# Kernel tuning notes

Hardware: AMD Instinct MI355X
Metric: run time of the kernel (lower is better)

The kernel has to match this reference:

```python
import jax, jax.numpy as jnp
from jax import lax
import numpy as np

B, H, W = 16, 512, 512
NBINS = 256
MARGIN_EYE = 12
BLUR_SIZE = 5
ALPHA_SKIN, ALPHA_EYE, ALPHA_LIP = 0.3, 0.8, 0.1


def de_norm(x):
    return jnp.clip((x + 1.0) * 0.5, 0.0, 1.0)


def renorm(x):
    return x * 2.0 - 1.0


def _match_channel(src, ref, w_s, w_r):
    # src/ref: (P,) pixel values in [0,255]; w_s/w_r: (P,) mask weights
    b_s = jnp.clip(src.astype(jnp.int32), 0, NBINS - 1)
    b_r = jnp.clip(ref.astype(jnp.int32), 0, NBINS - 1)
    h_s = jnp.zeros((NBINS,), src.dtype).at[b_s].add(w_s)   # masked histogram
    h_r = jnp.zeros((NBINS,), ref.dtype).at[b_r].add(w_r)
    cdf_s = jnp.cumsum(h_s) / jnp.maximum(jnp.sum(h_s), 1e-6)
    cdf_r = jnp.cumsum(h_r) / jnp.maximum(jnp.sum(h_r), 1e-6)
    # CDF-matching transfer table (equiv. of cal_trans in PSGAN/EleGANt)
    table = jnp.clip(jnp.searchsorted(cdf_r, cdf_s), 0, NBINS - 1).astype(src.dtype)
    return table[b_s]


def masked_his_match(image_s, image_r, mask_s, mask_r):
    # image: (3,H,W), mask: (1,H,W)
    s = de_norm(image_s) * 255.0 * mask_s
    r = de_norm(image_r) * 255.0 * mask_r
    w_s = mask_s.reshape(-1)
    w_r = mask_r.reshape(-1)
    matched = jax.vmap(_match_channel, in_axes=(0, 0, None, None))(
        s.reshape(3, -1), r.reshape(3, -1), w_s, w_r).reshape(s.shape)
    matched = jnp.where(mask_s > 0, matched, s)  # only masked pixels replaced
    return renorm(matched / 255.0)


def expand_area(mask, margin):
    # morphological dilation (max pool) of (1,H,W) mask
    k = 2 * margin + 1
    return lax.reduce_window(mask, 0.0, lax.max, (1, k, k), (1, 1, 1), 'SAME')


def mask_blur(mask, blur_size):
    # box blur; 'valid' mode: blurred support kept inside original mask
    k = blur_size
    s = lax.reduce_window(mask, 0.0, lax.add, (1, k, k), (1, 1, 1), 'SAME') / float(k * k)
    return s * mask


def generate_pgt(image_s, image_r, mask_s, mask_r, lms_s, lms_r):
    pgt = image_s
    # skin (channel 1)
    m = mask_s[1:2]
    pgt = (1.0 - m) * pgt + m * masked_his_match(image_s, image_r, m, mask_r[1:2])
    # neck (channel 4)
    m = mask_s[4:5]
    pgt = (1.0 - m) * pgt + m * masked_his_match(image_s, image_r, m, mask_r[4:5])
    # lip (channel 0)
    m = mask_s[0:1]
    pgt = (1.0 - m) * pgt + m * masked_his_match(image_s, image_r, m, mask_r[0:1])
    # eyes (channels 2,3), dilated and intersected with skin
    m_se = expand_area(jnp.sum(mask_s[2:4], axis=0, keepdims=True), MARGIN_EYE) * mask_s[1:2]
    m_re = expand_area(jnp.sum(mask_r[2:4], axis=0, keepdims=True), MARGIN_EYE) * mask_r[1:2]
    eye_match = masked_his_match(image_s, image_r, m_se, m_re)
    mb = mask_blur(m_se, BLUR_SIZE)
    pgt = (1.0 - mb) * pgt + mb * eye_match
    # fine_align (reconstructed, simplified: per-region alpha blend of reference,
    # landmark warp omitted -- helper source not provided)
    for m, a in ((mask_s[1:2], ALPHA_SKIN), (m_se, ALPHA_EYE), (mask_s[0:1], ALPHA_LIP)):
        pgt = (1.0 - a * m) * pgt + (a * m) * image_r
    return pgt


def setup_inputs() -> dict:
    key = jax.random.key(0)
    ks = jax.random.split(key, 6)
    sources = jax.random.uniform(ks[0], (B, 3, H, W), jnp.float32, -1.0, 1.0)
    targets = jax.random.uniform(ks[1], (B, 3, H, W), jnp.float32, -1.0, 1.0)
    mask_srcs = (jax.random.uniform(ks[2], (B, 5, H, W)) < 0.3).astype(jnp.float32)
    mask_tars = (jax.random.uniform(ks[3], (B, 5, H, W)) < 0.3).astype(jnp.float32)
    lms_srcs = jax.random.uniform(ks[4], (B, 68, 2), jnp.float32, 0.0, float(H))
    lms_tars = jax.random.uniform(ks[5], (B, 68, 2), jnp.float32, 0.0, float(H))
    return {"sources": sources, "targets": targets, "mask_srcs": mask_srcs,
            "mask_tars": mask_tars, "lms_srcs": lms_srcs, "lms_tars": lms_tars}


def reference(sources, targets, mask_srcs, mask_tars, lms_srcs, lms_tars):
    # vmap over batch replaces the per-sample Python loop of ComposePGT.forward
    return jax.vmap(generate_pgt)(sources, targets, mask_srcs, mask_tars, lms_srcs, lms_tars)
```

## Files before the change

### kernel.cpp

```cpp
#include <hip/hip_runtime.h>
#include <stdint.h>

#define BB 16
#define HH 512
#define WW 512
#define HW (HH*WW)
#define NB 256


__device__ __forceinline__ float denorm255(float x) {
    return fminf(fmaxf((x + 1.0f) * 0.5f, 0.0f), 1.0f) * 255.0f;
}
__device__ __forceinline__ float renorm_lut(int t) {
    return ((float)t / 255.0f) * 2.0f - 1.0f;
}
__device__ __forceinline__ uint32_t alignb(uint32_t hi, uint32_t lo, int r) {
    return (uint32_t)(((((uint64_t)hi) << 32) | lo) >> (8 * r));
}

__global__ void __launch_bounds__(256, 4) prep_hor_kernel(
    const float* __restrict__ ms, const float* __restrict__ mr,
    uint32_t* __restrict__ C, uint32_t* __restrict__ eh)
{
    int blk  = blockIdx.x;
    int side = blk >> 10;
    int rem  = blk & 1023;
    int b    = rem >> 6;
    int rg   = rem & 63;
    int r    = threadIdx.x >> 5;
    int c    = threadIdx.x & 31;
    int y    = (rg << 3) + r;

    const float* base = (side ? mr : ms) + (size_t)b * 5 * HW + (size_t)y * WW;

    float4 v[5][4];
    #pragma unroll
    for (int p = 0; p < 5; p++) {
        const float4* pp = (const float4*)(base + (size_t)p * HW);
        #pragma unroll
        for (int j = 0; j < 4; j++) v[p][j] = pp[4 * c + j];
    }

    uint32_t Wd[4], E[4];
    #pragma unroll
    for (int j = 0; j < 4; j++) {
        uint32_t wc = 0;
        #pragma unroll
        for (int k = 0; k < 4; k++) {
            float a0 = (&v[0][j].x)[k];
            float a1 = (&v[1][j].x)[k];
            float a2 = (&v[2][j].x)[k];
            float a3 = (&v[3][j].x)[k];
            float a4 = (&v[4][j].x)[k];
            uint32_t e  = (uint32_t)(a2 + a3);
            uint32_t pb = (a0 > 0.f ? 4u : 0u) | (a1 > 0.f ? 8u : 0u)
                        | (a4 > 0.f ? 16u : 0u);
            wc |= (e | pb) << (8 * k);
        }
        Wd[j] = wc;
        E[j]  = wc & 0x03030303u;
    }

    size_t plane = (size_t)(side * BB + b);
    uint32_t* Crow = C + plane * (HW / 4) + y * 128;
    *((uint4*)(Crow + 4 * c)) = make_uint4(Wd[0], Wd[1], Wd[2], Wd[3]);

    uint32_t Lw[3], Rw[3];
    #pragma unroll
    for (int i = 0; i < 3; i++) {
        uint32_t lv = __shfl_up(E[i + 1], 1, 32);
        Lw[i] = (c == 0) ? 0u : lv;
        uint32_t rv = __shfl_down(E[i], 1, 32);
        Rw[i] = (c == 31) ? 0u : rv;
    }
    uint32_t arr[10] = {Lw[0], Lw[1], Lw[2], E[0], E[1], E[2], E[3],
                        Rw[0], Rw[1], Rw[2]};

    uint32_t acc[4];
    #pragma unroll
    for (int k = 0; k < 4; k++) {
        const int b3 = 3 + k;
        uint32_t a = arr[b3];
        #pragma unroll
        for (int s = 1; s <= 12; s++) {
            int ai = s >> 2, rr = s & 3;
            uint32_t vp, vm;
            if (rr == 0) {
                vp = arr[b3 + ai];
                vm = arr[b3 - ai];
            } else {
                vp = alignb(arr[b3 + ai + 1], arr[b3 + ai], rr);
                int am = (s + 3) >> 2;
                vm = alignb(arr[b3 - am + 1], arr[b3 - am], 4 - rr);
            }
            a |= vp | vm;
        }
        acc[k] = a;
    }
    uint32_t* Erow = eh + plane * (HW / 4) + y * 128;
    *((uint4*)(Erow + 4 * c)) = make_uint4(acc[0], acc[1], acc[2], acc[3]);
}

__global__ void __launch_bounds__(256) ver_kernel(
    const uint32_t* __restrict__ eh, uint32_t* __restrict__ C)
{
    int t   = blockIdx.x * 256 + threadIdx.x;
    int sb  = t >> 12;
    int rem = t & 4095;
    int yg  = rem >> 5;
    int ck  = rem & 31;
    int y0  = yg << 2;
    const uint4* P = (const uint4*)(eh + (size_t)sb * (HW / 4));
    auto R = [&](int y) -> uint4 {
        uint4 z = {0, 0, 0, 0};
        if (y < 0 || y >= HH) return z;
        return P[y * 32 + ck];
    };
    uint4 core = {0, 0, 0, 0};
    #pragma unroll
    for (int yy = -9; yy <= 12; yy++) {
        uint4 r = R(y0 + yy);
        core.x |= r.x; core.y |= r.y; core.z |= r.z; core.w |= r.w;
    }
    uint4 b0 = R(y0 - 12), b1 = R(y0 - 11), b2 = R(y0 - 10);
    uint4 a0 = R(y0 + 13), a1 = R(y0 + 14), a2 = R(y0 + 15);

    uint4* C4 = (uint4*)(C + (size_t)sb * (HW / 4));
    #pragma unroll
    for (int i = 0; i < 4; i++) {
        uint4 v = core;
        if (i == 0) { v.x|=b0.x|b1.x|b2.x; v.y|=b0.y|b1.y|b2.y; v.z|=b0.z|b1.z|b2.z; v.w|=b0.w|b1.w|b2.w; }
        if (i == 1) { v.x|=b1.x|b2.x|a0.x; v.y|=b1.y|b2.y|a0.y; v.z|=b1.z|b2.z|a0.z; v.w|=b1.w|b2.w|a0.w; }
        if (i == 2) { v.x|=b2.x|a0.x|a1.x; v.y|=b2.y|a0.y|a1.y; v.z|=b2.z|a0.z|a1.z; v.w|=b2.w|a0.w|a1.w; }
        if (i == 3) { v.x|=a0.x|a1.x|a2.x; v.y|=a0.y|a1.y|a2.y; v.z|=a0.z|a1.z|a2.z; v.w|=a0.w|a1.w|a2.w; }
        int idx = (y0 + i) * 32 + ck;
        uint4 cw = C4[idx];
        #pragma unroll
        for (int q = 0; q < 4; q++) {
            uint32_t vv = (&v.x)[q];
            uint32_t cc = (&cw.x)[q];
            uint32_t t3 = vv & (vv >> 1) & 0x01010101u;
            vv -= t3;
            uint32_t m1b = (cc >> 3) & 0x01010101u;
            vv &= m1b * 255u;
            (&cw.x)[q] = cc | (vv << 5);
        }
        C4[idx] = cw;
    }
}

__global__ void __launch_bounds__(256) blur_kernel(
    const uint32_t* __restrict__ C, uint4* __restrict__ mbs)
{
    int t = blockIdx.x * 256 + threadIdx.x;
    int b = t >> 14;
    int rem = t & 16383;
    int y = rem >> 5;
    int c = rem & 31;
    const uint32_t* P = C + (size_t)b * (HW / 4);
    int c4 = c << 2;
    uint32_t s[6] = {0u, 0u, 0u, 0u, 0u, 0u};
    #pragma unroll
    for (int dy = -2; dy <= 2; dy++) {
        int yy = y + dy;
        if (yy < 0 || yy >= HH) continue;
        const uint32_t* rp = P + yy * 128;
        uint32_t l = (c > 0)  ? rp[c4 - 1] : 0u;
        uint4 m = *((const uint4*)(rp + c4));
        uint32_t rr = (c < 31) ? rp[c4 + 4] : 0u;
        s[0] += (l   >> 5) & 0x03030303u;
        s[1] += (m.x >> 5) & 0x03030303u;
        s[2] += (m.y >> 5) & 0x03030303u;
        s[3] += (m.z >> 5) & 0x03030303u;
        s[4] += (m.w >> 5) & 0x03030303u;
        s[5] += (rr  >> 5) & 0x03030303u;
    }
    uint4 o;
    #pragma unroll
    for (int k = 0; k < 4; k++) {
        uint32_t v = s[k + 1];
        v += alignb(s[k + 1], s[k],     2);
        v += alignb(s[k + 1], s[k],     3);
        v += alignb(s[k + 2], s[k + 1], 1);
        v += alignb(s[k + 2], s[k + 1], 2);
        (&o.x)[k] = v;
    }
    mbs[t] = o;
}

#define HB 32
__device__ __forceinline__ void hist4(int* h, uint32_t cw,
                                      float4 v0, float4 v1, float4 v2)
{
    float d0[4] = {denorm255(v0.x), denorm255(v0.y), denorm255(v0.z), denorm255(v0.w)};
    float d1[4] = {denorm255(v1.x), denorm255(v1.y), denorm255(v1.z), denorm255(v1.w)};
    float d2[4] = {denorm255(v2.x), denorm255(v2.y), denorm255(v2.z), denorm255(v2.w)};
    #pragma unroll
    for (int j = 0; j < 4; j++) {
        uint32_t pb = (cw >> (8 * j)) & 0xFFu;
        if (pb & 8u) {
            atomicAdd(&h[0 * NB + min((int)d0[j], 255)], 1);
            atomicAdd(&h[1 * NB + min((int)d1[j], 255)], 1);
            atomicAdd(&h[2 * NB + min((int)d2[j], 255)], 1);
        }
        if (pb & 16u) {
            atomicAdd(&h[3 * NB + min((int)d0[j], 255)], 1);
            atomicAdd(&h[4 * NB + min((int)d1[j], 255)], 1);
            atomicAdd(&h[5 * NB + min((int)d2[j], 255)], 1);
        }
        if (pb & 4u) {
            atomicAdd(&h[6 * NB + min((int)d0[j], 255)], 1);
            atomicAdd(&h[7 * NB + min((int)d1[j], 255)], 1);
            atomicAdd(&h[8 * NB + min((int)d2[j], 255)], 1);
        }
        int mei = (int)((pb >> 5) & 3u);
        if (mei) {
            float fm = (float)mei;
            atomicAdd(&h[ 9 * NB + min((int)(d0[j] * fm), 255)], mei);
            atomicAdd(&h[10 * NB + min((int)(d1[j] * fm), 255)], mei);
            atomicAdd(&h[11 * NB + min((int)(d2[j] * fm), 255)], mei);
        }
    }
}

__global__ void __launch_bounds__(256) hist_kernel(
    const float* __restrict__ src, const float* __restrict__ tgt,
    const uint32_t* __restrict__ C, int* __restrict__ hist)
{
    int bs  = blockIdx.x / HB;
    int blk = blockIdx.x % HB;
    int b = bs >> 1, side = bs & 1;
    const float* img = (side ? tgt : src) + (size_t)b * 3 * HW;
    const float4* i0 = (const float4*)(img);
    const float4* i1 = (const float4*)(img + HW);
    const float4* i2 = (const float4*)(img + 2 * (size_t)HW);
    const uint2* pc = (const uint2*)(C + (size_t)(side * BB + b) * (HW / 4));

    __shared__ int h[2][12 * NB];
    int* hw = h[threadIdx.x >> 7];
    for (int i = threadIdx.x; i < 2 * 12 * NB; i += 256) ((int*)h)[i] = 0;
    __syncthreads();

    for (int c = blk * 256 + threadIdx.x; c < HW / 8; c += HB * 256) {
        uint2 cw = pc[c];
        float4 a0 = i0[2 * c], b0 = i0[2 * c + 1];
        float4 a1 = i1[2 * c], b1 = i1[2 * c + 1];
        float4 a2 = i2[2 * c], b2 = i2[2 * c + 1];
        hist4(hw, cw.x, a0, a1, a2);
        hist4(hw, cw.y, b0, b1, b2);
    }
    __syncthreads();
    int* gh = hist + (size_t)bs * 12 * NB;
    for (int i = threadIdx.x; i < 12 * NB; i += 256) {
        int s = h[0][i] + h[1][i];
        if (s) atomicAdd(&gh[i], s);
    }
}

__global__ void __launch_bounds__(NB) table_kernel(
    const int* __restrict__ hist, uint8_t* __restrict__ table)
{
    int idx = blockIdx.x;
    int c = idx % 3; int rest = idx / 3; int rg = rest & 3; int b = rest >> 2;
    const int* hs = hist + ((size_t)((b * 2 + 0) * 4 + rg) * 3 + c) * NB;
    const int* hr = hist + ((size_t)((b * 2 + 1) * 4 + rg) * 3 + c) * NB;
    __shared__ int a[NB];
    __shared__ float cr[NB];
    int t = threadIdx.x;

    a[t] = hs[t];
    __syncthreads();
    for (int off = 1; off < NB; off <<= 1) {
        int v = (t >= off) ? a[t - off] : 0;
        __syncthreads();
        a[t] += v;
        __syncthreads();
    }
    int totS = a[NB - 1];
    int cumS = a[t];
    __syncthreads();

    a[t] = hr[t];
    __syncthreads();
    for (int off = 1; off < NB; off <<= 1) {
        int v = (t >= off) ? a[t - off] : 0;
        __syncthreads();
        a[t] += v;
        __syncthreads();
    }
    int totR = a[NB - 1];
    cr[t] = (float)a[t] / fmaxf((float)totR, 1e-6f);
    float v = (float)cumS / fmaxf((float)totS, 1e-6f);
    __syncthreads();

    int cnt = 0;
    for (int j = 0; j < NB; j++) cnt += (cr[j] < v) ? 1 : 0;
    table[(size_t)idx * NB + t] = (uint8_t)min(cnt, 255);
}

__device__ __forceinline__ void proc4(uint32_t cw, uint32_t qw,
    float4 x0, float4 x1, float4 x2, float4 r0, float4 r1, float4 r2,
    const uint8_t* tb, float4& o0, float4& o1, float4& o2)
{
    float X0[4] = {x0.x, x0.y, x0.z, x0.w};
    float X1[4] = {x1.x, x1.y, x1.z, x1.w};
    float X2[4] = {x2.x, x2.y, x2.z, x2.w};
    float R0[4] = {r0.x, r0.y, r0.z, r0.w};
    float R1[4] = {r1.x, r1.y, r1.z, r1.w};
    float R2[4] = {r2.x, r2.y, r2.z, r2.w};
    #pragma unroll
    for (int j = 0; j < 4; j++) {
        uint32_t pb = (cw >> (8 * j)) & 0xFFu;
        float q = (float)((qw >> (8 * j)) & 0xFFu);
        float m0f = (float)((pb >> 2) & 1u);
        float m1f = (float)((pb >> 3) & 1u);
        float m4f = (float)((pb >> 4) & 1u);
        float fm  = (float)((pb >> 5) & 3u);
        float d0 = denorm255(X0[j]), d1 = denorm255(X1[j]), d2 = denorm255(X2[j]);
        float p0 = X0[j], p1 = X1[j], p2 = X2[j];
        {
            float e0 = renorm_lut(tb[0 * NB + min((int)(d0 * m1f), 255)]);
            float e1 = renorm_lut(tb[1 * NB + min((int)(d1 * m1f), 255)]);
            float e2 = renorm_lut(tb[2 * NB + min((int)(d2 * m1f), 255)]);
            p0 = (1.0f - m1f) * p0 + m1f * e0;
            p1 = (1.0f - m1f) * p1 + m1f * e1;
            p2 = (1.0f - m1f) * p2 + m1f * e2;
        }
        {
            float e0 = renorm_lut(tb[3 * NB + min((int)(d0 * m4f), 255)]);
            float e1 = renorm_lut(tb[4 * NB + min((int)(d1 * m4f), 255)]);
            float e2 = renorm_lut(tb[5 * NB + min((int)(d2 * m4f), 255)]);
            p0 = (1.0f - m4f) * p0 + m4f * e0;
            p1 = (1.0f - m4f) * p1 + m4f * e1;
            p2 = (1.0f - m4f) * p2 + m4f * e2;
        }
        {
            float e0 = renorm_lut(tb[6 * NB + min((int)(d0 * m0f), 255)]);
            float e1 = renorm_lut(tb[7 * NB + min((int)(d1 * m0f), 255)]);
            float e2 = renorm_lut(tb[8 * NB + min((int)(d2 * m0f), 255)]);
            p0 = (1.0f - m0f) * p0 + m0f * e0;
            p1 = (1.0f - m0f) * p1 + m0f * e1;
            p2 = (1.0f - m0f) * p2 + m0f * e2;
        }
        {
            float mb = (q * (1.0f / 25.0f)) * fm;
            float e0 = renorm_lut(tb[ 9 * NB + min((int)(d0 * fm), 255)]);
            float e1 = renorm_lut(tb[10 * NB + min((int)(d1 * fm), 255)]);
            float e2 = renorm_lut(tb[11 * NB + min((int)(d2 * fm), 255)]);
            p0 = (1.0f - mb) * p0 + mb * e0;
            p1 = (1.0f - mb) * p1 + mb * e1;
            p2 = (1.0f - mb) * p2 + mb * e2;
        }
        float a = 0.3f * m1f;
        p0 = (1.0f - a) * p0 + a * R0[j];
        p1 = (1.0f - a) * p1 + a * R1[j];
        p2 = (1.0f - a) * p2 + a * R2[j];
        a = 0.8f * fm;
        p0 = (1.0f - a) * p0 + a * R0[j];
        p1 = (1.0f - a) * p1 + a * R1[j];
        p2 = (1.0f - a) * p2 + a * R2[j];
        a = 0.1f * m0f;
        p0 = (1.0f - a) * p0 + a * R0[j];
        p1 = (1.0f - a) * p1 + a * R1[j];
        p2 = (1.0f - a) * p2 + a * R2[j];
        (&o0.x)[j] = p0; (&o1.x)[j] = p1; (&o2.x)[j] = p2;
    }
}

__global__ void __launch_bounds__(256) compose_kernel(
    const float* __restrict__ src, const float* __restrict__ tgt,
    const uint32_t* __restrict__ C, const uint32_t* __restrict__ mbs,
    const uint8_t* __restrict__ table, float* __restrict__ out)
{
    int t = blockIdx.x * 256 + threadIdx.x;
    int b = t >> 15;
    int c = t & 32767;

    __shared__ uint8_t tb[12 * NB];
    {
        const uint32_t* gt = (const uint32_t*)(table + (size_t)b * 12 * NB);
        uint32_t* tw = (uint32_t*)tb;
        for (int i = threadIdx.x; i < 12 * NB / 4; i += 256) tw[i] = gt[i];
    }
    __syncthreads();

    const float4* s0 = (const float4*)(src + (size_t)b * 3 * HW);
    const float4* s1 = s0 + HW / 4;
    const float4* s2 = s1 + HW / 4;
    const float4* t0 = (const float4*)(tgt + (size_t)b * 3 * HW);
    const float4* t1 = t0 + HW / 4;
    const float4* t2 = t1 + HW / 4;
    const uint2* pc = (const uint2*)(C + (size_t)b * (HW / 4));
    const uint2* qc = (const uint2*)(mbs + (size_t)b * (HW / 4));
    float4* o0 = (float4*)(out + (size_t)b * 3 * HW);
    float4* o1 = o0 + HW / 4;
    float4* o2 = o1 + HW / 4;

    uint2 cw = pc[c];
    uint2 qw = qc[c];
    float4 xa0 = s0[2 * c], xb0 = s0[2 * c + 1];
    float4 xa1 = s1[2 * c], xb1 = s1[2 * c + 1];
    float4 xa2 = s2[2 * c], xb2 = s2[2 * c + 1];
    float4 ra0 = t0[2 * c], rb0 = t0[2 * c + 1];
    float4 ra1 = t1[2 * c], rb1 = t1[2 * c + 1];
    float4 ra2 = t2[2 * c], rb2 = t2[2 * c + 1];

    float4 oa0, oa1, oa2, ob0, ob1, ob2;
    proc4(cw.x, qw.x, xa0, xa1, xa2, ra0, ra1, ra2, tb, oa0, oa1, oa2);
    proc4(cw.y, qw.y, xb0, xb1, xb2, rb0, rb1, rb2, tb, ob0, ob1, ob2);

    o0[2 * c] = oa0; o0[2 * c + 1] = ob0;
    o1[2 * c] = oa1; o1[2 * c + 1] = ob1;
    o2[2 * c] = oa2; o2[2 * c + 1] = ob2;
}

extern "C" void kernel_launch(void* const* d_in, const int* in_sizes, int n_in,
                              void* d_out, int out_size, void* d_ws, size_t ws_size,
                              hipStream_t stream) {
    const float* src = (const float*)d_in[0];
    const float* tgt = (const float*)d_in[1];
    const float* ms  = (const float*)d_in[2];
    const float* mr  = (const float*)d_in[3];
    float* out = (float*)d_out;

    uint8_t* ws = (uint8_t*)d_ws;
    uint32_t* C   = (uint32_t*)(ws);
    uint32_t* eh  = (uint32_t*)(ws + (size_t)2 * BB * HW);
    uint32_t* mbs = (uint32_t*)(ws + (size_t)4 * BB * HW);
    int* hist     = (int*)(ws + (size_t)5 * BB * HW);
    uint8_t* table = ws + (size_t)5 * BB * HW + (size_t)2 * BB * 12 * NB * 4;

    hipMemsetAsync(hist, 0, (size_t)2 * BB * 12 * NB * sizeof(int), stream);

    prep_hor_kernel<<<2 * BB * 64, 256, 0, stream>>>(ms, mr, C, eh);
    ver_kernel<<<2 * BB * (HH / 4) * (WW / 16) / 256, 256, 0, stream>>>(eh, C);
    blur_kernel<<<BB * (HW / 16) / 256, 256, 0, stream>>>(C, (uint4*)mbs);
    hist_kernel<<<2 * BB * HB, 256, 0, stream>>>(src, tgt, C, hist);
    table_kernel<<<BB * 4 * 3, NB, 0, stream>>>(hist, table);
    compose_kernel<<<BB * (HW / 8) / 256, 256, 0, stream>>>(src, tgt, C, mbs, table, out);
}
```

Before: 330.7 us.

## Fuse mask prep, vertical dilation and blur into one LDS-tiled kernel

Replaces the three mask kernels (horizontal prep and dilation, vertical dilation, box blur) with one kernel. Each block handles a 36-row strip plus halo in shared memory, so the intermediate eh buffer and the re-read of C are no longer written to and read from global memory. It also skips loading mask planes that the halo rows do not need. The price is redundant halo loads and computation, only 480 blocks with large LDS use, and a blockIdx swizzle.

```diff
diff --git a/kernel.cpp b/kernel.cpp
--- a/kernel.cpp
+++ b/kernel.cpp
@@ -7,6 +7,11 @@
 #define HW (HH*WW)
 #define NB 256
 
+#define YC 36
+#define SROWS 64
+#define MROWS 40
+#define NYCH 15
+
 
 __device__ __forceinline__ float denorm255(float x) {
     return fminf(fmaxf((x + 1.0f) * 0.5f, 0.0f), 1.0f) * 255.0f;
@@ -18,174 +23,171 @@
     return (uint32_t)(((((uint64_t)hi) << 32) | lo) >> (8 * r));
 }
 
-__global__ void __launch_bounds__(256, 4) prep_hor_kernel(
+__global__ void __launch_bounds__(256) fused_mask_kernel(
     const float* __restrict__ ms, const float* __restrict__ mr,
-    uint32_t* __restrict__ C, uint32_t* __restrict__ eh)
-{
-    int blk  = blockIdx.x;
-    int side = blk >> 10;
-    int rem  = blk & 1023;
-    int b    = rem >> 6;
-    int rg   = rem & 63;
-    int r    = threadIdx.x >> 5;
-    int c    = threadIdx.x & 31;
-    int y    = (rg << 3) + r;
-
-    const float* base = (side ? mr : ms) + (size_t)b * 5 * HW + (size_t)y * WW;
-
-    float4 v[5][4];
-    #pragma unroll
-    for (int p = 0; p < 5; p++) {
-        const float4* pp = (const float4*)(base + (size_t)p * HW);
+    uint32_t* __restrict__ C, uint32_t* __restrict__ mbs)
+{
+    __shared__ uint32_t sHor[SROWS][128];
+    __shared__ uint32_t sMse[MROWS][129];
+
+    int blk  = (blockIdx.x & 7) * 60 + (blockIdx.x >> 3);
+    int ych  = blk % NYCH;
+    int sb   = blk / NYCH;
+    int side = sb >> 4;
+    int b    = sb & 15;
+    int y0   = ych * YC;
+
+    const float* base = (side ? mr : ms) + (size_t)b * 5 * HW;
+    int r0 = threadIdx.x >> 5;
+    int c  = threadIdx.x & 31;
+
+    for (int it = 0; it < 8; ++it) {
+        int L  = r0 + 8 * it;
+        int gy = y0 - 14 + L;
+        bool inimg = (gy >= 0 && gy < HH);
+        bool m1row = inimg && (L >= 12 && L < 52);
+        bool owned = inimg && (L >= 14 && L < 50);
+
+        float4 v[5][4];
         #pragma unroll
-        for (int j = 0; j < 4; j++) v[p][j] = pp[4 * c + j];
-    }
-
-    uint32_t Wd[4], E[4];
-    #pragma unroll
-    for (int j = 0; j < 4; j++) {
-        uint32_t wc = 0;
+        for (int p = 0; p < 5; p++)
+            #pragma unroll
+            for (int j = 0; j < 4; j++) v[p][j] = make_float4(0.f, 0.f, 0.f, 0.f);
+
+        const float* rowp = base + (size_t)gy * WW + 16 * c;
+        if (inimg) {
+            const float4* p2 = (const float4*)(rowp + 2 * (size_t)HW);
+            const float4* p3 = (const float4*)(rowp + 3 * (size_t)HW);
+            #pragma unroll
+            for (int j = 0; j < 4; j++) { v[2][j] = p2[j]; v[3][j] = p3[j]; }
+            if (m1row) {
+                const float4* p1 = (const float4*)(rowp + (size_t)HW);
+                #pragma unroll
+                for (int j = 0; j < 4; j++) v[1][j] = p1[j];
+            }
+            if (owned) {
+                const float4* p0 = (const float4*)(rowp);
+                const float4* p4 = (const float4*)(rowp + 4 * (size_t)HW);
+                #pragma unroll
+                for (int j = 0; j < 4; j++) { v[0][j] = p0[j]; v[4][j] = p4[j]; }
+            }
+        }
+
+        uint32_t Wd[4], E[4];
+        #pragma unroll
+        for (int j = 0; j < 4; j++) {
+            uint32_t wc = 0;
+            #pragma unroll
+            for (int k = 0; k < 4; k++) {
+                float a0 = (&v[0][j].x)[k];
+                float a1 = (&v[1][j].x)[k];
+                float a2 = (&v[2][j].x)[k];
+                float a3 = (&v[3][j].x)[k];
+                float a4 = (&v[4][j].x)[k];
+                uint32_t e  = (uint32_t)(a2 + a3);
+                uint32_t pb = (a0 > 0.f ? 4u : 0u) | (a1 > 0.f ? 8u : 0u)
+                            | (a4 > 0.f ? 16u : 0u);
+                wc |= (e | pb) << (8 * k);
+            }
+            Wd[j] = wc;
+            E[j]  = wc & 0x03030303u;
+        }
+
+        uint32_t Lw[3], Rw[3];
+        #pragma unroll
+        for (int i = 0; i < 3; i++) {
+            uint32_t lv = __shfl_up(E[i + 1], 1, 32);
+            Lw[i] = (c == 0) ? 0u : lv;
+            uint32_t rv = __shfl_down(E[i], 1, 32);
+            Rw[i] = (c == 31) ? 0u : rv;
+        }
+        uint32_t arr[10] = {Lw[0], Lw[1], Lw[2], E[0], E[1], E[2], E[3],
+                            Rw[0], Rw[1], Rw[2]};
         #pragma unroll
         for (int k = 0; k < 4; k++) {
-            float a0 = (&v[0][j].x)[k];
-            float a1 = (&v[1][j].x)[k];
-            float a2 = (&v[2][j].x)[k];
-            float a3 = (&v[3][j].x)[k];
-            float a4 = (&v[4][j].x)[k];
-            uint32_t e  = (uint32_t)(a2 + a3);
-            uint32_t pb = (a0 > 0.f ? 4u : 0u) | (a1 > 0.f ? 8u : 0u)
-                        | (a4 > 0.f ? 16u : 0u);
-            wc |= (e | pb) << (8 * k);
-        }
-        Wd[j] = wc;
-        E[j]  = wc & 0x03030303u;
-    }
-
-    size_t plane = (size_t)(side * BB + b);
-    uint32_t* Crow = C + plane * (HW / 4) + y * 128;
-    *((uint4*)(Crow + 4 * c)) = make_uint4(Wd[0], Wd[1], Wd[2], Wd[3]);
-
-    uint32_t Lw[3], Rw[3];
-    #pragma unroll
-    for (int i = 0; i < 3; i++) {
-        uint32_t lv = __shfl_up(E[i + 1], 1, 32);
-        Lw[i] = (c == 0) ? 0u : lv;
-        uint32_t rv = __shfl_down(E[i], 1, 32);
-        Rw[i] = (c == 31) ? 0u : rv;
-    }
-    uint32_t arr[10] = {Lw[0], Lw[1], Lw[2], E[0], E[1], E[2], E[3],
-                        Rw[0], Rw[1], Rw[2]};
-
-    uint32_t acc[4];
-    #pragma unroll
-    for (int k = 0; k < 4; k++) {
-        const int b3 = 3 + k;
-        uint32_t a = arr[b3];
-        #pragma unroll
-        for (int s = 1; s <= 12; s++) {
-            int ai = s >> 2, rr = s & 3;
-            uint32_t vp, vm;
-            if (rr == 0) {
-                vp = arr[b3 + ai];
-                vm = arr[b3 - ai];
-            } else {
-                vp = alignb(arr[b3 + ai + 1], arr[b3 + ai], rr);
-                int am = (s + 3) >> 2;
-                vm = alignb(arr[b3 - am + 1], arr[b3 - am], 4 - rr);
-            }
-            a |= vp | vm;
-        }
-        acc[k] = a;
-    }
-    uint32_t* Erow = eh + plane * (HW / 4) + y * 128;
-    *((uint4*)(Erow + 4 * c)) = make_uint4(acc[0], acc[1], acc[2], acc[3]);
-}
-
-__global__ void __launch_bounds__(256) ver_kernel(
-    const uint32_t* __restrict__ eh, uint32_t* __restrict__ C)
-{
-    int t   = blockIdx.x * 256 + threadIdx.x;
-    int sb  = t >> 12;
-    int rem = t & 4095;
-    int yg  = rem >> 5;
-    int ck  = rem & 31;
-    int y0  = yg << 2;
-    const uint4* P = (const uint4*)(eh + (size_t)sb * (HW / 4));
-    auto R = [&](int y) -> uint4 {
-        uint4 z = {0, 0, 0, 0};
-        if (y < 0 || y >= HH) return z;
-        return P[y * 32 + ck];
-    };
-    uint4 core = {0, 0, 0, 0};
-    #pragma unroll
-    for (int yy = -9; yy <= 12; yy++) {
-        uint4 r = R(y0 + yy);
-        core.x |= r.x; core.y |= r.y; core.z |= r.z; core.w |= r.w;
-    }
-    uint4 b0 = R(y0 - 12), b1 = R(y0 - 11), b2 = R(y0 - 10);
-    uint4 a0 = R(y0 + 13), a1 = R(y0 + 14), a2 = R(y0 + 15);
-
-    uint4* C4 = (uint4*)(C + (size_t)sb * (HW / 4));
-    #pragma unroll
-    for (int i = 0; i < 4; i++) {
-        uint4 v = core;
-        if (i == 0) { v.x|=b0.x|b1.x|b2.x; v.y|=b0.y|b1.y|b2.y; v.z|=b0.z|b1.z|b2.z; v.w|=b0.w|b1.w|b2.w; }
-        if (i == 1) { v.x|=b1.x|b2.x|a0.x; v.y|=b1.y|b2.y|a0.y; v.z|=b1.z|b2.z|a0.z; v.w|=b1.w|b2.w|a0.w; }
-        if (i == 2) { v.x|=b2.x|a0.x|a1.x; v.y|=b2.y|a0.y|a1.y; v.z|=b2.z|a0.z|a1.z; v.w|=b2.w|a0.w|a1.w; }
-        if (i == 3) { v.x|=a0.x|a1.x|a2.x; v.y|=a0.y|a1.y|a2.y; v.z|=a0.z|a1.z|a2.z; v.w|=a0.w|a1.w|a2.w; }
-        int idx = (y0 + i) * 32 + ck;
-        uint4 cw = C4[idx];
-        #pragma unroll
-        for (int q = 0; q < 4; q++) {
-            uint32_t vv = (&v.x)[q];
-            uint32_t cc = (&cw.x)[q];
+            const int b3 = 3 + k;
+            uint32_t a = arr[b3];
+            #pragma unroll
+            for (int s = 1; s <= 12; s++) {
+                int ai = s >> 2, rrs = s & 3;
+                uint32_t vp, vm;
+                if (rrs == 0) {
+                    vp = arr[b3 + ai];
+                    vm = arr[b3 - ai];
+                } else {
+                    vp = alignb(arr[b3 + ai + 1], arr[b3 + ai], rrs);
+                    int am = (s + 3) >> 2;
+                    vm = alignb(arr[b3 - am + 1], arr[b3 - am], 4 - rrs);
+                }
+                a |= vp | vm;
+            }
+            sHor[L][4 * c + k] = Wd[k] | (a << 5);
+        }
+    }
+    __syncthreads();
+
+    {
+        int w  = threadIdx.x & 127;
+        int mg = threadIdx.x >> 7;
+        for (int k = 0; k < 20; ++k) {
+            int m = mg * 20 + k;
+            uint32_t o = 0;
+            #pragma unroll
+            for (int dy = 0; dy < 25; ++dy) o |= sHor[m + dy][w];
+            uint32_t vv = (o >> 5) & 0x03030303u;
             uint32_t t3 = vv & (vv >> 1) & 0x01010101u;
             vv -= t3;
-            uint32_t m1b = (cc >> 3) & 0x01010101u;
-            vv &= m1b * 255u;
-            (&cw.x)[q] = cc | (vv << 5);
-        }
-        C4[idx] = cw;
-    }
-}
-
-__global__ void __launch_bounds__(256) blur_kernel(
-    const uint32_t* __restrict__ C, uint4* __restrict__ mbs)
-{
-    int t = blockIdx.x * 256 + threadIdx.x;
-    int b = t >> 14;
-    int rem = t & 16383;
-    int y = rem >> 5;
-    int c = rem & 31;
-    const uint32_t* P = C + (size_t)b * (HW / 4);
-    int c4 = c << 2;
-    uint32_t s[6] = {0u, 0u, 0u, 0u, 0u, 0u};
-    #pragma unroll
-    for (int dy = -2; dy <= 2; dy++) {
-        int yy = y + dy;
-        if (yy < 0 || yy >= HH) continue;
-        const uint32_t* rp = P + yy * 128;
-        uint32_t l = (c > 0)  ? rp[c4 - 1] : 0u;
-        uint4 m = *((const uint4*)(rp + c4));
-        uint32_t rr = (c < 31) ? rp[c4 + 4] : 0u;
-        s[0] += (l   >> 5) & 0x03030303u;
-        s[1] += (m.x >> 5) & 0x03030303u;
-        s[2] += (m.y >> 5) & 0x03030303u;
-        s[3] += (m.z >> 5) & 0x03030303u;
-        s[4] += (m.w >> 5) & 0x03030303u;
-        s[5] += (rr  >> 5) & 0x03030303u;
-    }
-    uint4 o;
-    #pragma unroll
-    for (int k = 0; k < 4; k++) {
-        uint32_t v = s[k + 1];
-        v += alignb(s[k + 1], s[k],     2);
-        v += alignb(s[k + 1], s[k],     3);
-        v += alignb(s[k + 2], s[k + 1], 1);
-        v += alignb(s[k + 2], s[k + 1], 2);
-        (&o.x)[k] = v;
-    }
-    mbs[t] = o;
+            uint32_t m1 = (sHor[m + 12][w] >> 3) & 0x01010101u;
+            vv &= m1 * 3u;
+            sMse[m][w] = vv;
+        }
+    }
+    __syncthreads();
+
+    {
+        int ck = threadIdx.x & 31;
+        int rr = threadIdx.x >> 5;
+        size_t plane = (size_t)(side * BB + b);
+        uint32_t* Cp = C + plane * (HW / 4);
+        uint32_t* Mp = mbs + (size_t)b * (HW / 4);
+        for (int o = rr; o < YC; o += 8) {
+            int gy = y0 + o;
+            if (gy >= HH) break;
+            uint4 cw;
+            #pragma unroll
+            for (int q = 0; q < 4; q++) {
+                uint32_t b5 = sHor[14 + o][4 * ck + q] & 0x1F1F1F1Fu;
+                uint32_t mv = sMse[o + 2][4 * ck + q];
+                (&cw.x)[q] = b5 | (mv << 5);
+            }
+            *((uint4*)(Cp + (size_t)gy * 128 + 4 * ck)) = cw;
+
+            if (side == 0) {
+                uint32_t s[6] = {0u, 0u, 0u, 0u, 0u, 0u};
+                #pragma unroll
+                for (int dy = 0; dy < 5; dy++) {
+                    const uint32_t* rp = sMse[o + dy];
+                    if (ck > 0)  s[0] += rp[4 * ck - 1];
+                    s[1] += rp[4 * ck + 0];
+                    s[2] += rp[4 * ck + 1];
+                    s[3] += rp[4 * ck + 2];
+                    s[4] += rp[4 * ck + 3];
+                    if (ck < 31) s[5] += rp[4 * ck + 4];
+                }
+                uint4 ob;
+                #pragma unroll
+                for (int k = 0; k < 4; k++) {
+                    uint32_t vv = s[k + 1];
+                    vv += alignb(s[k + 1], s[k],     2);
+                    vv += alignb(s[k + 1], s[k],     3);
+                    vv += alignb(s[k + 2], s[k + 1], 1);
+                    vv += alignb(s[k + 2], s[k + 1], 2);
+                    (&ob.x)[k] = vv;
+                }
+                *((uint4*)(Mp + (size_t)gy * 128 + 4 * ck)) = ob;
+            }
+        }
+    }
 }
 
 #define HB 32
@@ -425,16 +427,13 @@
 
     uint8_t* ws = (uint8_t*)d_ws;
     uint32_t* C   = (uint32_t*)(ws);
-    uint32_t* eh  = (uint32_t*)(ws + (size_t)2 * BB * HW);
     uint32_t* mbs = (uint32_t*)(ws + (size_t)4 * BB * HW);
     int* hist     = (int*)(ws + (size_t)5 * BB * HW);
     uint8_t* table = ws + (size_t)5 * BB * HW + (size_t)2 * BB * 12 * NB * 4;
 
     hipMemsetAsync(hist, 0, (size_t)2 * BB * 12 * NB * sizeof(int), stream);
 
-    prep_hor_kernel<<<2 * BB * 64, 256, 0, stream>>>(ms, mr, C, eh);
-    ver_kernel<<<2 * BB * (HH / 4) * (WW / 16) / 256, 256, 0, stream>>>(eh, C);
-    blur_kernel<<<BB * (HW / 16) / 256, 256, 0, stream>>>(C, (uint4*)mbs);
+    fused_mask_kernel<<<2 * BB * NYCH, 256, 0, stream>>>(ms, mr, C, mbs);
     hist_kernel<<<2 * BB * HB, 256, 0, stream>>>(src, tgt, C, hist);
     table_kernel<<<BB * 4 * 3, NB, 0, stream>>>(hist, table);
     compose_kernel<<<BB * (HW / 8) / 256, 256, 0, stream>>>(src, tgt, C, mbs, table, out);
```

Result: no change. 335.1 us (+1.4%).
